# Performance work log

Measured on AMD Instinct MI355X. Metric: run time of the kernel, lower is better.

## Reference

```python
import jax, jax.numpy as jnp
import numpy as np

EULER = 0.5772156649015329  # Euler-Mascheroni constant


def _expi_neg(t):
    """Ei(t) for t < 0, via Ei(t) = -E1(-t).

    E1 uses the power series for x < 8 and the asymptotic expansion for x >= 8.
    This replaces the scipy.special.expi CPU round-trip of the original module.
    """
    x = -t  # x > 0
    # --- series branch (x < 8): E1(x) = -gamma - ln(x) + sum_{k>=1} (-1)^{k+1} x^k/(k*k!)
    xs = jnp.minimum(x, 8.0)
    s = jnp.zeros_like(xs)
    term = xs  # (-1)^{k+1} xs^k / k!  starting at k=1
    for k in range(1, 31):
        s = s + term / k
        term = term * (-xs) / (k + 1)
    e1_small = -EULER - jnp.log(xs) + s
    # --- asymptotic branch (x >= 8): E1(x) ~ e^{-x}/x * sum_n (-1)^n n! / x^n
    xl = jnp.maximum(x, 8.0)
    a = jnp.ones_like(xl)
    acc = jnp.ones_like(xl)
    for n in range(1, 9):
        a = a * (-n) / xl
        acc = acc + a
    e1_large = jnp.exp(-xl) / xl * acc
    e1 = jnp.where(x < 8.0, e1_small, e1_large)
    return -e1


def _li(v):
    # logarithmic integral li(v) = Ei(ln v); constant w.r.t. params (scipy detaches in torch)
    return jax.lax.stop_gradient(_expi_neg(jnp.log(v)))


def _phi(u, var2, var3, var4, var5):
    log_term = jnp.log(1.0 - u)
    li_term = _li(1.0 - u)
    return (var2 / log_term
            + var3 * li_term
            + var4 * ((1.0 - u) / log_term - li_term)
            + var5 * ((1.0 - u) * (log_term + 1.0) / (2.0 * log_term ** 2) - li_term / 2.0))


def setup_inputs() -> dict:
    key = jax.random.key(0)
    B, L, D = 262144, 64, 32
    hidden = [128, 128, 64]
    ks = jax.random.split(key, 16)
    u = jax.random.uniform(ks[0], (B, L), dtype=jnp.float32, minval=1e-4, maxval=1.0 - 1e-4)
    dims = [L] + hidden + [D]
    inp = {"u": u}
    for i in range(4):
        inp[f"W{i}"] = jax.random.normal(ks[1 + 2 * i], (dims[i], dims[i + 1]), dtype=jnp.float32) / np.sqrt(dims[i]).astype(np.float32)
        inp[f"b{i}"] = jnp.zeros((dims[i + 1],), dtype=jnp.float32)
    for j in range(1, 7):
        inp[f"var{j}"] = jax.random.normal(ks[8 + j], (1, D), dtype=jnp.float32) * 0.1
    return inp


def reference(u, W0, b0, W1, b1, W2, b2, W3, b3, var1, var2, var3, var4, var5, var6):
    # MLP: three Linear+ReLU blocks then final Linear to dim_data
    h = u
    for W, b in ((W0, b0), (W1, b1), (W2, b2)):
        h = jax.nn.relu(h @ W + b)
    net = h @ W3 + b3  # (B, dim_data)
    D = net.shape[1]
    ud = u[:, :D]
    # spline corrections
    p01 = -4.0 * ud ** 5 + 5.0 * ud ** 4
    corr1 = jnp.nan_to_num(p01 * (var1 + _phi(ud, var2, var3, var4, var5)), nan=0.0)
    corr2 = var6 * (ud ** 3 - 2.0 * ud ** 2 + ud)
    net_tif = jax.nn.relu(net + corr1 + corr2)
    # inverse TIF activation: ((1 - u^2)/2)^{-x}
    return jnp.power((1.0 - ud ** 2) / 2.0, -net_tif)
```

## Files before the change

### kernel.cpp

```cpp
#include <hip/hip_runtime.h>
#include <hip/hip_bf16.h>
#include <math.h>

#define PITCH_H 136
#define LN2_F 0.69314718055994531f

typedef _Float16 half8 __attribute__((ext_vector_type(8)));
typedef __attribute__((ext_vector_type(4))) float f32x4;
typedef __attribute__((ext_vector_type(8))) short short8;

__global__ void prep_weights(const float* __restrict__ W0, const float* __restrict__ W1,
                             const float* __restrict__ W2, const float* __restrict__ W3,
                             short* __restrict__ ws) {
    int e = blockIdx.x * 256 + threadIdx.x;
    const float* W; int N, NT, base, ul;
    if (e < 1024)      { W = W0; N = 128; NT = 8; base = 0;     ul = e; }
    else if (e < 3072) { W = W1; N = 128; NT = 8; base = 8192;  ul = e - 1024; }
    else if (e < 4096) { W = W2; N = 64;  NT = 4; base = 24576; ul = e - 3072; }
    else if (e < 4352) { W = W3; N = 32;  NT = 2; base = 32768; ul = e - 4096; }
    else return;
    const int cp = ul >> 6, lane = ul & 63;
    const int s = cp / NT, ct = cp % NT;
    const int k0 = s * 32 + (lane >> 4) * 8;
    const int n = ct * 16 + (lane & 15);
    union { half8 h; short8 s; } v;
#pragma unroll
    for (int j = 0; j < 8; ++j) v.h[j] = (_Float16)W[(size_t)(k0 + j) * N + n];
    *(short8*)(ws + base + cp * 512 + lane * 8) = v.s;
}

template <int K, int N>
__device__ __forceinline__ void layer_frag2(const half8* __restrict__ wf,
                                            const float* __restrict__ bias,
                                            const half8 (&af)[2][4], int lane, int m,
                                            f32x4 (&acc)[2][8]) {
    constexpr int NK = K / 32, NT = N / 16;
#pragma unroll
    for (int ct = 0; ct < NT; ++ct) {
        float b = bias[ct * 16 + m];
        acc[0][ct] = f32x4{b, b, b, b};
        acc[1][ct] = f32x4{b, b, b, b};
    }
#pragma unroll
    for (int s = 0; s < NK; ++s) {
#pragma unroll
        for (int ct = 0; ct < NT; ++ct) {
            half8 bh = wf[(size_t)(s * NT + ct) * 64 + lane];
            acc[0][ct] = __builtin_amdgcn_mfma_f32_16x16x32_f16(af[0][s], bh, acc[0][ct], 0, 0, 0);
            acc[1][ct] = __builtin_amdgcn_mfma_f32_16x16x32_f16(af[1][s], bh, acc[1][ct], 0, 0, 0);
        }
    }
}

template <int K>
__device__ __forceinline__ void load_a_lds(const _Float16* __restrict__ lw, int m, int q,
                                           half8 af[4]) {
    const _Float16* rp = lw + m * PITCH_H + q * 8;
#pragma unroll
    for (int s = 0; s < K / 32; ++s) af[s] = *(const half8*)(rp + s * 32);
}

template <int N>
__device__ __forceinline__ void store_d_lds(_Float16* __restrict__ lw, int m, int q,
                                            const f32x4* acc, bool relu) {
#pragma unroll
    for (int ct = 0; ct < N / 16; ++ct) {
#pragma unroll
        for (int r = 0; r < 4; ++r) {
            float v = acc[ct][r];
            if (relu) v = fmaxf(v, 0.0f);
            lw[(q * 4 + r) * PITCH_H + ct * 16 + m] = (_Float16)v;
        }
    }
}

__global__ __launch_bounds__(256, 2) void mlp_phi_mfma(
    const float* __restrict__ u,
    const float* __restrict__ b0, const float* __restrict__ b1,
    const float* __restrict__ b2, const float* __restrict__ b3,
    const short* __restrict__ ws,
    const float* __restrict__ var1, const float* __restrict__ var2,
    const float* __restrict__ var3, const float* __restrict__ var4,
    const float* __restrict__ var5, const float* __restrict__ var6,
    float* __restrict__ out) {
    __shared__ __align__(16) _Float16 lds[4 * 32 * PITCH_H];
    const int t = threadIdx.x, lane = t & 63, wave = t >> 6;
    const int m = lane & 15, q = lane >> 4;
    _Float16* lw = lds + wave * 32 * PITCH_H;
    const size_t row0 = (size_t)blockIdx.x * 128 + wave * 32;

    const half8* wf0 = (const half8*)(ws);
    const half8* wf1 = (const half8*)(ws + 8192);
    const half8* wf2 = (const half8*)(ws + 24576);
    const half8* wf3 = (const half8*)(ws + 32768);

    half8 af[2][4];
    f32x4 acc[2][8];

#pragma unroll
    for (int mt = 0; mt < 2; ++mt) {
        const float* up = u + (row0 + mt * 16 + m) * 64;
#pragma unroll
        for (int s = 0; s < 2; ++s) {
            float4 v0 = *(const float4*)(up + s * 32 + q * 8);
            float4 v1 = *(const float4*)(up + s * 32 + q * 8 + 4);
            half8 a;
            a[0] = (_Float16)v0.x; a[1] = (_Float16)v0.y;
            a[2] = (_Float16)v0.z; a[3] = (_Float16)v0.w;
            a[4] = (_Float16)v1.x; a[5] = (_Float16)v1.y;
            a[6] = (_Float16)v1.z; a[7] = (_Float16)v1.w;
            af[mt][s] = a;
        }
    }
    layer_frag2<64, 128>(wf0, b0, af, lane, m, acc);
#pragma unroll
    for (int mt = 0; mt < 2; ++mt) store_d_lds<128>(lw + mt * 16 * PITCH_H, m, q, acc[mt], true);

#pragma unroll
    for (int mt = 0; mt < 2; ++mt) load_a_lds<128>(lw + mt * 16 * PITCH_H, m, q, af[mt]);
    layer_frag2<128, 128>(wf1, b1, af, lane, m, acc);
#pragma unroll
    for (int mt = 0; mt < 2; ++mt) store_d_lds<128>(lw + mt * 16 * PITCH_H, m, q, acc[mt], true);

#pragma unroll
    for (int mt = 0; mt < 2; ++mt) load_a_lds<128>(lw + mt * 16 * PITCH_H, m, q, af[mt]);
    layer_frag2<128, 64>(wf2, b2, af, lane, m, acc);
#pragma unroll
    for (int mt = 0; mt < 2; ++mt) store_d_lds<64>(lw + mt * 16 * PITCH_H, m, q, acc[mt], true);

#pragma unroll
    for (int mt = 0; mt < 2; ++mt) load_a_lds<64>(lw + mt * 16 * PITCH_H, m, q, af[mt]);

    float ue[2][8];
#pragma unroll
    for (int mt = 0; mt < 2; ++mt)
#pragma unroll
        for (int ot = 0; ot < 2; ++ot)
#pragma unroll
            for (int r = 0; r < 4; ++r)
                ue[mt][ot * 4 + r] = u[(row0 + mt * 16 + q * 4 + r) * 64 + ot * 16 + m];

    layer_frag2<64, 32>(wf3, b3, af, lane, m, acc);

#pragma unroll
    for (int ot = 0; ot < 2; ++ot) {
        const int d = ot * 16 + m;
        const float v1 = var1[d], v2 = var2[d], v3 = var3[d],
                    v4 = var4[d], v6 = var6[d];
        const float v5h = 0.5f * var5[d];
        const float c3 = v3 - v4 - v5h;
#pragma unroll
        for (int mt = 0; mt < 2; ++mt) {
#pragma unroll
            for (int r = 0; r < 4; ++r) {
                const size_t row = row0 + mt * 16 + q * 4 + r;
                const float net = acc[mt][ot][r];
                const float ud = ue[mt][ot * 4 + r];

                const float omu = 1.0f - ud;
                const float lt = __log2f(omu) * LN2_F;
                const float x = -lt;

                const float e1s = -__log2f(x) * LN2_F
                    + (-0.57721566f + x * (0.99999193f + x * (-0.24991055f
                    + x * (0.05519968f + x * (-0.00976004f + x * 0.00107857f)))));
                const float num = 0.2677737343f + x * (8.6347608925f + x * (18.0590169730f
                    + x * (8.5733287401f + x)));
                const float den = 3.9584969228f + x * (21.0996530827f + x * (25.6329561486f
                    + x * (9.5733223454f + x)));
                const float e1l = __expf(-x) * num * __builtin_amdgcn_rcpf(x * den);
                const float li = -((x < 1.0f) ? e1s : e1l);

                const float rl = __builtin_amdgcn_rcpf(lt);
                const float phi = fmaf(v4, omu, v2) * rl
                                + (v5h * omu * (lt + 1.0f)) * rl * rl
                                + c3 * li;

                const float ud2 = ud * ud;
                const float ud4 = ud2 * ud2;
                const float p01 = ud4 * fmaf(-4.0f, ud, 5.0f);
                const float corr1 = p01 * (v1 + phi);
                const float d1 = ud - 1.0f;
                const float corr2 = v6 * ud * d1 * d1;

                const float nt = fmaxf(net + corr1 + corr2, 0.0f);
                const float base = fmaf(-0.5f, ud2, 0.5f);
                out[row * 32 + d] = __builtin_amdgcn_exp2f(-nt * __log2f(base));
            }
        }
    }
}

extern "C" void kernel_launch(void* const* d_in, const int* in_sizes, int n_in,
                              void* d_out, int out_size, void* d_ws, size_t ws_size,
                              hipStream_t stream) {
    const float* u    = (const float*)d_in[0];
    const float* W0   = (const float*)d_in[1];
    const float* b0   = (const float*)d_in[2];
    const float* W1   = (const float*)d_in[3];
    const float* b1   = (const float*)d_in[4];
    const float* W2   = (const float*)d_in[5];
    const float* b2   = (const float*)d_in[6];
    const float* W3   = (const float*)d_in[7];
    const float* b3   = (const float*)d_in[8];
    const float* var1 = (const float*)d_in[9];
    const float* var2 = (const float*)d_in[10];
    const float* var3 = (const float*)d_in[11];
    const float* var4 = (const float*)d_in[12];
    const float* var5 = (const float*)d_in[13];
    const float* var6 = (const float*)d_in[14];
    float* out = (float*)d_out;
    short* ws = (short*)d_ws;

    prep_weights<<<dim3(17), dim3(256), 0, stream>>>(W0, W1, W2, W3, ws);

    const int B = in_sizes[0] / 64;
    const int blocks = B / 128;
    mlp_phi_mfma<<<dim3(blocks), dim3(256), 0, stream>>>(
        u, b0, b1, b2, b3, ws,
        var1, var2, var3, var4, var5, var6, out);
}
```

Baseline: 158.4 us.

## Stage fp16 weights in LDS with persistent 512-thread blocks

Converts the kernel to a persistent grid of up to 256 blocks of 512 threads that loop over 256-row chunks. Each block copies the prepacked fp16 weights into LDS once and hoists biases and var-derived constants into registers, so MFMA B-fragments are read from LDS instead of global/L2 on every tile. LDS use rises to about 139 KB per block, which can allow only one block per CU and caps the grid at 256 blocks. That limits occupancy and latency hiding, and the weight copy is a fixed startup cost per block.

```diff
diff --git a/kernel.cpp b/kernel.cpp
--- a/kernel.cpp
+++ b/kernel.cpp
@@ -4,6 +4,10 @@
 
 #define PITCH_H 136
 #define LN2_F 0.69314718055994531f
+#define WS_SHORTS 34816
+#define WS_BYTES  69632
+#define ACT_BYTES (8 * 32 * PITCH_H * 2)
+#define LDS_TOTAL (WS_BYTES + ACT_BYTES)
 
 typedef _Float16 half8 __attribute__((ext_vector_type(8)));
 typedef __attribute__((ext_vector_type(4))) float f32x4;
@@ -30,14 +34,14 @@
 }
 
 template <int K, int N>
-__device__ __forceinline__ void layer_frag2(const half8* __restrict__ wf,
-                                            const float* __restrict__ bias,
-                                            const half8 (&af)[2][4], int lane, int m,
+__device__ __forceinline__ void layer_frag2(const half8* wf,
+                                            const float* bias,
+                                            const half8 (&af)[2][4], int lane,
                                             f32x4 (&acc)[2][8]) {
     constexpr int NK = K / 32, NT = N / 16;
 #pragma unroll
     for (int ct = 0; ct < NT; ++ct) {
-        float b = bias[ct * 16 + m];
+        float b = bias[ct];
         acc[0][ct] = f32x4{b, b, b, b};
         acc[1][ct] = f32x4{b, b, b, b};
     }
@@ -45,7 +49,7 @@
     for (int s = 0; s < NK; ++s) {
 #pragma unroll
         for (int ct = 0; ct < NT; ++ct) {
-            half8 bh = wf[(size_t)(s * NT + ct) * 64 + lane];
+            half8 bh = wf[(s * NT + ct) * 64 + lane];
             acc[0][ct] = __builtin_amdgcn_mfma_f32_16x16x32_f16(af[0][s], bh, acc[0][ct], 0, 0, 0);
             acc[1][ct] = __builtin_amdgcn_mfma_f32_16x16x32_f16(af[1][s], bh, acc[1][ct], 0, 0, 0);
         }
@@ -74,7 +78,7 @@
     }
 }
 
-__global__ __launch_bounds__(256, 2) void mlp_phi_mfma(
+__global__ __launch_bounds__(512, 2) void mlp_phi_mfma(
     const float* __restrict__ u,
     const float* __restrict__ b0, const float* __restrict__ b1,
     const float* __restrict__ b2, const float* __restrict__ b3,
@@ -82,110 +86,141 @@
     const float* __restrict__ var1, const float* __restrict__ var2,
     const float* __restrict__ var3, const float* __restrict__ var4,
     const float* __restrict__ var5, const float* __restrict__ var6,
-    float* __restrict__ out) {
-    __shared__ __align__(16) _Float16 lds[4 * 32 * PITCH_H];
+    float* __restrict__ out, int nchunks) {
+    extern __shared__ __align__(16) char smem[];
+    short* wsl = (short*)smem;
+    _Float16* act = (_Float16*)(smem + WS_BYTES);
+
     const int t = threadIdx.x, lane = t & 63, wave = t >> 6;
     const int m = lane & 15, q = lane >> 4;
-    _Float16* lw = lds + wave * 32 * PITCH_H;
-    const size_t row0 = (size_t)blockIdx.x * 128 + wave * 32;
-
-    const half8* wf0 = (const half8*)(ws);
-    const half8* wf1 = (const half8*)(ws + 8192);
-    const half8* wf2 = (const half8*)(ws + 24576);
-    const half8* wf3 = (const half8*)(ws + 32768);
+
+#pragma unroll 1
+    for (int i = t; i < WS_SHORTS / 8; i += 512)
+        ((short8*)wsl)[i] = ((const short8*)ws)[i];
+
+    float bb0[8], bb1[8], bb2[4], bb3[2];
+#pragma unroll
+    for (int ct = 0; ct < 8; ++ct) bb0[ct] = b0[ct * 16 + m];
+#pragma unroll
+    for (int ct = 0; ct < 8; ++ct) bb1[ct] = b1[ct * 16 + m];
+#pragma unroll
+    for (int ct = 0; ct < 4; ++ct) bb2[ct] = b2[ct * 16 + m];
+#pragma unroll
+    for (int ct = 0; ct < 2; ++ct) bb3[ct] = b3[ct * 16 + m];
+
+    float ev1[2], ev2[2], ev4[2], ev6[2], ev5h[2], ec3[2];
+#pragma unroll
+    for (int ot = 0; ot < 2; ++ot) {
+        const int d = ot * 16 + m;
+        ev1[ot] = var1[d]; ev2[ot] = var2[d]; ev4[ot] = var4[d]; ev6[ot] = var6[d];
+        ev5h[ot] = 0.5f * var5[d];
+        ec3[ot] = var3[d] - ev4[ot] - ev5h[ot];
+    }
+
+    __syncthreads();
+
+    const half8* wf0 = (const half8*)(wsl);
+    const half8* wf1 = (const half8*)(wsl + 8192);
+    const half8* wf2 = (const half8*)(wsl + 24576);
+    const half8* wf3 = (const half8*)(wsl + 32768);
+    _Float16* lw = act + wave * 32 * PITCH_H;
 
     half8 af[2][4];
     f32x4 acc[2][8];
 
-#pragma unroll
-    for (int mt = 0; mt < 2; ++mt) {
-        const float* up = u + (row0 + mt * 16 + m) * 64;
-#pragma unroll
-        for (int s = 0; s < 2; ++s) {
-            float4 v0 = *(const float4*)(up + s * 32 + q * 8);
-            float4 v1 = *(const float4*)(up + s * 32 + q * 8 + 4);
-            half8 a;
-            a[0] = (_Float16)v0.x; a[1] = (_Float16)v0.y;
-            a[2] = (_Float16)v0.z; a[3] = (_Float16)v0.w;
-            a[4] = (_Float16)v1.x; a[5] = (_Float16)v1.y;
-            a[6] = (_Float16)v1.z; a[7] = (_Float16)v1.w;
-            af[mt][s] = a;
-        }
-    }
-    layer_frag2<64, 128>(wf0, b0, af, lane, m, acc);
-#pragma unroll
-    for (int mt = 0; mt < 2; ++mt) store_d_lds<128>(lw + mt * 16 * PITCH_H, m, q, acc[mt], true);
-
-#pragma unroll
-    for (int mt = 0; mt < 2; ++mt) load_a_lds<128>(lw + mt * 16 * PITCH_H, m, q, af[mt]);
-    layer_frag2<128, 128>(wf1, b1, af, lane, m, acc);
-#pragma unroll
-    for (int mt = 0; mt < 2; ++mt) store_d_lds<128>(lw + mt * 16 * PITCH_H, m, q, acc[mt], true);
-
-#pragma unroll
-    for (int mt = 0; mt < 2; ++mt) load_a_lds<128>(lw + mt * 16 * PITCH_H, m, q, af[mt]);
-    layer_frag2<128, 64>(wf2, b2, af, lane, m, acc);
-#pragma unroll
-    for (int mt = 0; mt < 2; ++mt) store_d_lds<64>(lw + mt * 16 * PITCH_H, m, q, acc[mt], true);
-
-#pragma unroll
-    for (int mt = 0; mt < 2; ++mt) load_a_lds<64>(lw + mt * 16 * PITCH_H, m, q, af[mt]);
-
-    float ue[2][8];
-#pragma unroll
-    for (int mt = 0; mt < 2; ++mt)
-#pragma unroll
-        for (int ot = 0; ot < 2; ++ot)
-#pragma unroll
-            for (int r = 0; r < 4; ++r)
-                ue[mt][ot * 4 + r] = u[(row0 + mt * 16 + q * 4 + r) * 64 + ot * 16 + m];
-
-    layer_frag2<64, 32>(wf3, b3, af, lane, m, acc);
-
-#pragma unroll
-    for (int ot = 0; ot < 2; ++ot) {
-        const int d = ot * 16 + m;
-        const float v1 = var1[d], v2 = var2[d], v3 = var3[d],
-                    v4 = var4[d], v6 = var6[d];
-        const float v5h = 0.5f * var5[d];
-        const float c3 = v3 - v4 - v5h;
+#pragma unroll 1
+    for (int c = blockIdx.x; c < nchunks; c += gridDim.x) {
+        const size_t row0 = (size_t)c * 256 + wave * 32;
+
 #pragma unroll
         for (int mt = 0; mt < 2; ++mt) {
-#pragma unroll
-            for (int r = 0; r < 4; ++r) {
-                const size_t row = row0 + mt * 16 + q * 4 + r;
-                const float net = acc[mt][ot][r];
-                const float ud = ue[mt][ot * 4 + r];
-
-                const float omu = 1.0f - ud;
-                const float lt = __log2f(omu) * LN2_F;
-                const float x = -lt;
-
-                const float e1s = -__log2f(x) * LN2_F
-                    + (-0.57721566f + x * (0.99999193f + x * (-0.24991055f
-                    + x * (0.05519968f + x * (-0.00976004f + x * 0.00107857f)))));
-                const float num = 0.2677737343f + x * (8.6347608925f + x * (18.0590169730f
-                    + x * (8.5733287401f + x)));
-                const float den = 3.9584969228f + x * (21.0996530827f + x * (25.6329561486f
-                    + x * (9.5733223454f + x)));
-                const float e1l = __expf(-x) * num * __builtin_amdgcn_rcpf(x * den);
-                const float li = -((x < 1.0f) ? e1s : e1l);
-
-                const float rl = __builtin_amdgcn_rcpf(lt);
-                const float phi = fmaf(v4, omu, v2) * rl
-                                + (v5h * omu * (lt + 1.0f)) * rl * rl
-                                + c3 * li;
-
-                const float ud2 = ud * ud;
-                const float ud4 = ud2 * ud2;
-                const float p01 = ud4 * fmaf(-4.0f, ud, 5.0f);
-                const float corr1 = p01 * (v1 + phi);
-                const float d1 = ud - 1.0f;
-                const float corr2 = v6 * ud * d1 * d1;
-
-                const float nt = fmaxf(net + corr1 + corr2, 0.0f);
-                const float base = fmaf(-0.5f, ud2, 0.5f);
-                out[row * 32 + d] = __builtin_amdgcn_exp2f(-nt * __log2f(base));
+            const float* up = u + (row0 + mt * 16 + m) * 64;
+#pragma unroll
+            for (int s = 0; s < 2; ++s) {
+                float4 v0 = *(const float4*)(up + s * 32 + q * 8);
+                float4 v1 = *(const float4*)(up + s * 32 + q * 8 + 4);
+                half8 a;
+                a[0] = (_Float16)v0.x; a[1] = (_Float16)v0.y;
+                a[2] = (_Float16)v0.z; a[3] = (_Float16)v0.w;
+                a[4] = (_Float16)v1.x; a[5] = (_Float16)v1.y;
+                a[6] = (_Float16)v1.z; a[7] = (_Float16)v1.w;
+                af[mt][s] = a;
+            }
+        }
+        layer_frag2<64, 128>(wf0, bb0, af, lane, acc);
+#pragma unroll
+        for (int mt = 0; mt < 2; ++mt) store_d_lds<128>(lw + mt * 16 * PITCH_H, m, q, acc[mt], true);
+
+#pragma unroll
+        for (int mt = 0; mt < 2; ++mt) load_a_lds<128>(lw + mt * 16 * PITCH_H, m, q, af[mt]);
+        layer_frag2<128, 128>(wf1, bb1, af, lane, acc);
+#pragma unroll
+        for (int mt = 0; mt < 2; ++mt) store_d_lds<128>(lw + mt * 16 * PITCH_H, m, q, acc[mt], true);
+
+#pragma unroll
+        for (int mt = 0; mt < 2; ++mt) load_a_lds<128>(lw + mt * 16 * PITCH_H, m, q, af[mt]);
+        layer_frag2<128, 64>(wf2, bb2, af, lane, acc);
+#pragma unroll
+        for (int mt = 0; mt < 2; ++mt) store_d_lds<64>(lw + mt * 16 * PITCH_H, m, q, acc[mt], true);
+
+#pragma unroll
+        for (int mt = 0; mt < 2; ++mt) load_a_lds<64>(lw + mt * 16 * PITCH_H, m, q, af[mt]);
+
+        float ue[2][8];
+#pragma unroll
+        for (int mt = 0; mt < 2; ++mt)
+#pragma unroll
+            for (int ot = 0; ot < 2; ++ot)
+#pragma unroll
+                for (int r = 0; r < 4; ++r)
+                    ue[mt][ot * 4 + r] = u[(row0 + mt * 16 + q * 4 + r) * 64 + ot * 16 + m];
+
+        layer_frag2<64, 32>(wf3, bb3, af, lane, acc);
+
+#pragma unroll
+        for (int ot = 0; ot < 2; ++ot) {
+            const int d = ot * 16 + m;
+            const float v1 = ev1[ot], v2 = ev2[ot], v4 = ev4[ot], v6 = ev6[ot];
+            const float v5h = ev5h[ot];
+            const float c3 = ec3[ot];
+#pragma unroll
+            for (int mt = 0; mt < 2; ++mt) {
+#pragma unroll
+                for (int r = 0; r < 4; ++r) {
+                    const size_t row = row0 + mt * 16 + q * 4 + r;
+                    const float net = acc[mt][ot][r];
+                    const float ud = ue[mt][ot * 4 + r];
+
+                    const float omu = 1.0f - ud;
+                    const float lt = __log2f(omu) * LN2_F;
+                    const float x = -lt;
+
+                    const float e1s = -__log2f(x) * LN2_F
+                        + (-0.57721566f + x * (0.99999193f + x * (-0.24991055f
+                        + x * (0.05519968f + x * (-0.00976004f + x * 0.00107857f)))));
+                    const float num = 0.2677737343f + x * (8.6347608925f + x * (18.0590169730f
+                        + x * (8.5733287401f + x)));
+                    const float den = 3.9584969228f + x * (21.0996530827f + x * (25.6329561486f
+                        + x * (9.5733223454f + x)));
+                    const float e1l = __expf(-x) * num * __builtin_amdgcn_rcpf(x * den);
+                    const float li = -((x < 1.0f) ? e1s : e1l);
+
+                    const float rl = __builtin_amdgcn_rcpf(lt);
+                    const float phi = fmaf(v4, omu, v2) * rl
+                                    + (v5h * omu * (lt + 1.0f)) * rl * rl
+                                    + c3 * li;
+
+                    const float ud2 = ud * ud;
+                    const float ud4 = ud2 * ud2;
+                    const float p01 = ud4 * fmaf(-4.0f, ud, 5.0f);
+                    const float corr1 = p01 * (v1 + phi);
+                    const float d1 = ud - 1.0f;
+                    const float corr2 = v6 * ud * d1 * d1;
+
+                    const float nt = fmaxf(net + corr1 + corr2, 0.0f);
+                    const float base = fmaf(-0.5f, ud2, 0.5f);
+                    out[row * 32 + d] = __builtin_amdgcn_exp2f(-nt * __log2f(base));
+                }
             }
         }
     }
@@ -214,9 +249,13 @@
 
     prep_weights<<<dim3(17), dim3(256), 0, stream>>>(W0, W1, W2, W3, ws);
 
+    hipFuncSetAttribute(reinterpret_cast<const void*>(mlp_phi_mfma),
+                        hipFuncAttributeMaxDynamicSharedMemorySize, LDS_TOTAL);
+
     const int B = in_sizes[0] / 64;
-    const int blocks = B / 128;
-    mlp_phi_mfma<<<dim3(blocks), dim3(256), 0, stream>>>(
+    const int nchunks = B / 256;
+    const int nblocks = nchunks < 256 ? nchunks : 256;
+    mlp_phi_mfma<<<dim3(nblocks), dim3(512), LDS_TOTAL, stream>>>(
         u, b0, b1, b2, b3, ws,
-        var1, var2, var3, var4, var5, var6, out);
-}
+        var1, var2, var3, var4, var5, var6, out, nchunks);
+}
```

New measurement: 150.2 us. -5.2%, faster.

## Use transposed LDS reads, double-buffered weight prefetch, and higher occupancy

Applied to the files above, without the earlier changes.

Swaps the padded row-major LDS staging between layers for a fragment-blocked layout that is read back with ds_read_b64_tr_b16, so each lane gets its A fragment from packed 64-bit stores and transposed loads rather than scalar half stores. Weight fragments are now prefetched one K-step ahead into two register buffers, and biases and spline parameters are loaded once at kernel start. Float-to-half conversion uses packed cvt_pkrtz, which rounds toward zero instead of to nearest. Launch bounds move from 2 to 4 blocks per CU, which caps register use and may cause spills given the larger register footprint.

```diff
diff --git a/kernel.cpp b/kernel.cpp
--- a/kernel.cpp
+++ b/kernel.cpp
@@ -2,10 +2,11 @@
 #include <hip/hip_bf16.h>
 #include <math.h>
 
-#define PITCH_H 136
 #define LN2_F 0.69314718055994531f
 
 typedef _Float16 half8 __attribute__((ext_vector_type(8)));
+typedef _Float16 h4_t __attribute__((ext_vector_type(4)));
+typedef __fp16 pk2_t __attribute__((ext_vector_type(2)));
 typedef __attribute__((ext_vector_type(4))) float f32x4;
 typedef __attribute__((ext_vector_type(8))) short short8;
 
@@ -29,52 +30,83 @@
     *(short8*)(ws + base + cp * 512 + lane * 8) = v.s;
 }
 
+#define REGION_HALFS 2048
+
+__device__ __forceinline__ void lds_fence() {
+    asm volatile("s_waitcnt lgkmcnt(0)" ::: "memory");
+}
+
+template <int K>
+__device__ __forceinline__ void load_a_tr(const _Float16* region, unsigned lane_off,
+                                          half8 af[4]) {
+    const unsigned base = (unsigned)(uintptr_t)region + lane_off;
+#pragma unroll
+    for (int s = 0; s < K / 32; ++s) {
+        h4_t lo, hi;
+        asm volatile("ds_read_b64_tr_b16 %0, %2\n\t"
+                     "ds_read_b64_tr_b16 %1, %2 offset:128"
+                     : "=&v"(lo), "=&v"(hi)
+                     : "v"(base + (unsigned)(s * 1024))
+                     : "memory");
+        af[s] = __builtin_shufflevector(lo, hi, 0, 1, 2, 3, 4, 5, 6, 7);
+    }
+}
+
+template <int N>
+__device__ __forceinline__ void store_d_tr(_Float16* __restrict__ region, int m, int q,
+                                           const f32x4* acc, bool relu) {
+    const int base = (m >> 2) * 64 + (m & 3) * 16 + q * 4;
+#pragma unroll
+    for (int ct = 0; ct < N / 16; ++ct) {
+        f32x4 v = acc[ct];
+        float a0 = relu ? fmaxf(v[0], 0.0f) : v[0];
+        float a1 = relu ? fmaxf(v[1], 0.0f) : v[1];
+        float a2 = relu ? fmaxf(v[2], 0.0f) : v[2];
+        float a3 = relu ? fmaxf(v[3], 0.0f) : v[3];
+        pk2_t p0 = __builtin_amdgcn_cvt_pkrtz(a0, a1);
+        pk2_t p1 = __builtin_amdgcn_cvt_pkrtz(a2, a3);
+        h4_t h = {(_Float16)p0[0], (_Float16)p0[1], (_Float16)p1[0], (_Float16)p1[1]};
+        *(h4_t*)(region + ct * 256 + base) = h;
+    }
+}
+
+template <int NT>
+__device__ __forceinline__ void preload_b(const half8* __restrict__ wf, int lane,
+                                          half8 (&b)[8]) {
+#pragma unroll
+    for (int ct = 0; ct < NT; ++ct) b[ct] = wf[ct * 64 + lane];
+}
+
 template <int K, int N>
 __device__ __forceinline__ void layer_frag2(const half8* __restrict__ wf,
-                                            const float* __restrict__ bias,
-                                            const half8 (&af)[2][4], int lane, int m,
-                                            f32x4 (&acc)[2][8]) {
+                                            const float* bias,
+                                            const half8 (&af)[2][4], int lane,
+                                            f32x4 (&acc)[2][8],
+                                            half8 (&ba)[8], half8 (&bb)[8]) {
     constexpr int NK = K / 32, NT = N / 16;
 #pragma unroll
     for (int ct = 0; ct < NT; ++ct) {
-        float b = bias[ct * 16 + m];
+        float b = bias[ct];
         acc[0][ct] = f32x4{b, b, b, b};
         acc[1][ct] = f32x4{b, b, b, b};
     }
 #pragma unroll
     for (int s = 0; s < NK; ++s) {
+        half8 (&bc)[8] = (s & 1) ? bb : ba;
+        half8 (&bn)[8] = (s & 1) ? ba : bb;
+        if (s + 1 < NK) {
+#pragma unroll
+            for (int ct = 0; ct < NT; ++ct) bn[ct] = wf[((s + 1) * NT + ct) * 64 + lane];
+        }
 #pragma unroll
         for (int ct = 0; ct < NT; ++ct) {
-            half8 bh = wf[(size_t)(s * NT + ct) * 64 + lane];
-            acc[0][ct] = __builtin_amdgcn_mfma_f32_16x16x32_f16(af[0][s], bh, acc[0][ct], 0, 0, 0);
-            acc[1][ct] = __builtin_amdgcn_mfma_f32_16x16x32_f16(af[1][s], bh, acc[1][ct], 0, 0, 0);
-        }
-    }
-}
-
-template <int K>
-__device__ __forceinline__ void load_a_lds(const _Float16* __restrict__ lw, int m, int q,
-                                           half8 af[4]) {
-    const _Float16* rp = lw + m * PITCH_H + q * 8;
-#pragma unroll
-    for (int s = 0; s < K / 32; ++s) af[s] = *(const half8*)(rp + s * 32);
-}
-
-template <int N>
-__device__ __forceinline__ void store_d_lds(_Float16* __restrict__ lw, int m, int q,
-                                            const f32x4* acc, bool relu) {
-#pragma unroll
-    for (int ct = 0; ct < N / 16; ++ct) {
-#pragma unroll
-        for (int r = 0; r < 4; ++r) {
-            float v = acc[ct][r];
-            if (relu) v = fmaxf(v, 0.0f);
-            lw[(q * 4 + r) * PITCH_H + ct * 16 + m] = (_Float16)v;
-        }
-    }
-}
-
-__global__ __launch_bounds__(256, 2) void mlp_phi_mfma(
+            acc[0][ct] = __builtin_amdgcn_mfma_f32_16x16x32_f16(af[0][s], bc[ct], acc[0][ct], 0, 0, 0);
+            acc[1][ct] = __builtin_amdgcn_mfma_f32_16x16x32_f16(af[1][s], bc[ct], acc[1][ct], 0, 0, 0);
+        }
+    }
+}
+
+__global__ __launch_bounds__(256, 4) void mlp_phi_mfma(
     const float* __restrict__ u,
     const float* __restrict__ b0, const float* __restrict__ b1,
     const float* __restrict__ b2, const float* __restrict__ b3,
@@ -83,10 +115,11 @@
     const float* __restrict__ var3, const float* __restrict__ var4,
     const float* __restrict__ var5, const float* __restrict__ var6,
     float* __restrict__ out) {
-    __shared__ __align__(16) _Float16 lds[4 * 32 * PITCH_H];
+    __shared__ __align__(16) _Float16 lds[4 * 2 * REGION_HALFS];
     const int t = threadIdx.x, lane = t & 63, wave = t >> 6;
     const int m = lane & 15, q = lane >> 4;
-    _Float16* lw = lds + wave * 32 * PITCH_H;
+    _Float16* lw = lds + wave * 2 * REGION_HALFS;
+    const unsigned lane_rd = (unsigned)(q * 256 + m * 8);
     const size_t row0 = (size_t)blockIdx.x * 128 + wave * 32;
 
     const half8* wf0 = (const half8*)(ws);
@@ -94,8 +127,28 @@
     const half8* wf2 = (const half8*)(ws + 24576);
     const half8* wf3 = (const half8*)(ws + 32768);
 
+    float bb0v[8], bb1v[8], bb2v[4], bb3v[2];
+#pragma unroll
+    for (int ct = 0; ct < 8; ++ct) bb0v[ct] = b0[ct * 16 + m];
+#pragma unroll
+    for (int ct = 0; ct < 8; ++ct) bb1v[ct] = b1[ct * 16 + m];
+#pragma unroll
+    for (int ct = 0; ct < 4; ++ct) bb2v[ct] = b2[ct * 16 + m];
+#pragma unroll
+    for (int ct = 0; ct < 2; ++ct) bb3v[ct] = b3[ct * 16 + m];
+
+    float ev1[2], ev2[2], ev4[2], ev6[2], ev5h[2], ec3[2];
+#pragma unroll
+    for (int ot = 0; ot < 2; ++ot) {
+        const int d = ot * 16 + m;
+        ev1[ot] = var1[d]; ev2[ot] = var2[d]; ev4[ot] = var4[d]; ev6[ot] = var6[d];
+        ev5h[ot] = 0.5f * var5[d];
+        ec3[ot] = var3[d] - ev4[ot] - ev5h[ot];
+    }
+
     half8 af[2][4];
     f32x4 acc[2][8];
+    half8 ba[8], bb[8];
 
 #pragma unroll
     for (int mt = 0; mt < 2; ++mt) {
@@ -104,32 +157,43 @@
         for (int s = 0; s < 2; ++s) {
             float4 v0 = *(const float4*)(up + s * 32 + q * 8);
             float4 v1 = *(const float4*)(up + s * 32 + q * 8 + 4);
-            half8 a;
-            a[0] = (_Float16)v0.x; a[1] = (_Float16)v0.y;
-            a[2] = (_Float16)v0.z; a[3] = (_Float16)v0.w;
-            a[4] = (_Float16)v1.x; a[5] = (_Float16)v1.y;
-            a[6] = (_Float16)v1.z; a[7] = (_Float16)v1.w;
-            af[mt][s] = a;
-        }
-    }
-    layer_frag2<64, 128>(wf0, b0, af, lane, m, acc);
-#pragma unroll
-    for (int mt = 0; mt < 2; ++mt) store_d_lds<128>(lw + mt * 16 * PITCH_H, m, q, acc[mt], true);
-
-#pragma unroll
-    for (int mt = 0; mt < 2; ++mt) load_a_lds<128>(lw + mt * 16 * PITCH_H, m, q, af[mt]);
-    layer_frag2<128, 128>(wf1, b1, af, lane, m, acc);
-#pragma unroll
-    for (int mt = 0; mt < 2; ++mt) store_d_lds<128>(lw + mt * 16 * PITCH_H, m, q, acc[mt], true);
-
-#pragma unroll
-    for (int mt = 0; mt < 2; ++mt) load_a_lds<128>(lw + mt * 16 * PITCH_H, m, q, af[mt]);
-    layer_frag2<128, 64>(wf2, b2, af, lane, m, acc);
-#pragma unroll
-    for (int mt = 0; mt < 2; ++mt) store_d_lds<64>(lw + mt * 16 * PITCH_H, m, q, acc[mt], true);
-
-#pragma unroll
-    for (int mt = 0; mt < 2; ++mt) load_a_lds<64>(lw + mt * 16 * PITCH_H, m, q, af[mt]);
+            pk2_t p0 = __builtin_amdgcn_cvt_pkrtz(v0.x, v0.y);
+            pk2_t p1 = __builtin_amdgcn_cvt_pkrtz(v0.z, v0.w);
+            pk2_t p2 = __builtin_amdgcn_cvt_pkrtz(v1.x, v1.y);
+            pk2_t p3 = __builtin_amdgcn_cvt_pkrtz(v1.z, v1.w);
+            af[mt][s] = half8{(_Float16)p0[0], (_Float16)p0[1], (_Float16)p1[0], (_Float16)p1[1],
+                              (_Float16)p2[0], (_Float16)p2[1], (_Float16)p3[0], (_Float16)p3[1]};
+        }
+    }
+    preload_b<8>(wf0, lane, ba);
+    layer_frag2<64, 128>(wf0, bb0v, af, lane, acc, ba, bb);
+#pragma unroll
+    for (int mt = 0; mt < 2; ++mt) store_d_tr<128>(lw + mt * REGION_HALFS, m, q, acc[mt], true);
+
+    preload_b<8>(wf1, lane, ba);
+    lds_fence();
+    load_a_tr<128>(lw, lane_rd, af[0]);
+    load_a_tr<128>(lw + REGION_HALFS, lane_rd, af[1]);
+    lds_fence();
+    __builtin_amdgcn_sched_barrier(0);
+    layer_frag2<128, 128>(wf1, bb1v, af, lane, acc, ba, bb);
+#pragma unroll
+    for (int mt = 0; mt < 2; ++mt) store_d_tr<128>(lw + mt * REGION_HALFS, m, q, acc[mt], true);
+
+    preload_b<4>(wf2, lane, ba);
+    lds_fence();
+    load_a_tr<128>(lw, lane_rd, af[0]);
+    load_a_tr<128>(lw + REGION_HALFS, lane_rd, af[1]);
+    lds_fence();
+    __builtin_amdgcn_sched_barrier(0);
+    layer_frag2<128, 64>(wf2, bb2v, af, lane, acc, ba, bb);
+#pragma unroll
+    for (int mt = 0; mt < 2; ++mt) store_d_tr<64>(lw + mt * REGION_HALFS, m, q, acc[mt], true);
+
+    preload_b<2>(wf3, lane, ba);
+    lds_fence();
+    load_a_tr<64>(lw, lane_rd, af[0]);
+    load_a_tr<64>(lw + REGION_HALFS, lane_rd, af[1]);
 
     float ue[2][8];
 #pragma unroll
@@ -140,15 +204,16 @@
             for (int r = 0; r < 4; ++r)
                 ue[mt][ot * 4 + r] = u[(row0 + mt * 16 + q * 4 + r) * 64 + ot * 16 + m];
 
-    layer_frag2<64, 32>(wf3, b3, af, lane, m, acc);
+    lds_fence();
+    __builtin_amdgcn_sched_barrier(0);
+    layer_frag2<64, 32>(wf3, bb3v, af, lane, acc, ba, bb);
 
 #pragma unroll
     for (int ot = 0; ot < 2; ++ot) {
         const int d = ot * 16 + m;
-        const float v1 = var1[d], v2 = var2[d], v3 = var3[d],
-                    v4 = var4[d], v6 = var6[d];
-        const float v5h = 0.5f * var5[d];
-        const float c3 = v3 - v4 - v5h;
+        const float v1 = ev1[ot], v2 = ev2[ot], v4 = ev4[ot], v6 = ev6[ot];
+        const float v5h = ev5h[ot];
+        const float c3 = ec3[ot];
 #pragma unroll
         for (int mt = 0; mt < 2; ++mt) {
 #pragma unroll
```

Result: slower. 175.9 us (+11.0%).

## Keep weight slices in registers with persistent grid and column-split waves

Applied to the files above, without the earlier changes.

Restructures the MLP kernel so each wave owns a fixed slice of output columns and holds its slice of all four weight matrices in registers. A persistent grid of up to 1024 blocks loops over 32-row chunks, which removes the per-block weight reloads from global memory. Activations pass between layers through LDS with a tiled layout read by transposing ds_read_b64_tr_b16 loads. The cost is three block-wide barriers per layer step and less per-wave work to hide latency, since the four waves now split columns of the same rows.

```diff
diff --git a/kernel.cpp b/kernel.cpp
--- a/kernel.cpp
+++ b/kernel.cpp
@@ -2,10 +2,12 @@
 #include <hip/hip_bf16.h>
 #include <math.h>
 
-#define PITCH_H 136
 #define LN2_F 0.69314718055994531f
+#define REGION_HALFS 2048
 
 typedef _Float16 half8 __attribute__((ext_vector_type(8)));
+typedef _Float16 h4_t __attribute__((ext_vector_type(4)));
+typedef __fp16 pk2_t __attribute__((ext_vector_type(2)));
 typedef __attribute__((ext_vector_type(4))) float f32x4;
 typedef __attribute__((ext_vector_type(8))) short short8;
 
@@ -29,49 +31,32 @@
     *(short8*)(ws + base + cp * 512 + lane * 8) = v.s;
 }
 
-template <int K, int N>
-__device__ __forceinline__ void layer_frag2(const half8* __restrict__ wf,
-                                            const float* __restrict__ bias,
-                                            const half8 (&af)[2][4], int lane, int m,
-                                            f32x4 (&acc)[2][8]) {
-    constexpr int NK = K / 32, NT = N / 16;
-#pragma unroll
-    for (int ct = 0; ct < NT; ++ct) {
-        float b = bias[ct * 16 + m];
-        acc[0][ct] = f32x4{b, b, b, b};
-        acc[1][ct] = f32x4{b, b, b, b};
-    }
-#pragma unroll
-    for (int s = 0; s < NK; ++s) {
-#pragma unroll
-        for (int ct = 0; ct < NT; ++ct) {
-            half8 bh = wf[(size_t)(s * NT + ct) * 64 + lane];
-            acc[0][ct] = __builtin_amdgcn_mfma_f32_16x16x32_f16(af[0][s], bh, acc[0][ct], 0, 0, 0);
-            acc[1][ct] = __builtin_amdgcn_mfma_f32_16x16x32_f16(af[1][s], bh, acc[1][ct], 0, 0, 0);
-        }
-    }
-}
-
-template <int K>
-__device__ __forceinline__ void load_a_lds(const _Float16* __restrict__ lw, int m, int q,
-                                           half8 af[4]) {
-    const _Float16* rp = lw + m * PITCH_H + q * 8;
-#pragma unroll
-    for (int s = 0; s < K / 32; ++s) af[s] = *(const half8*)(rp + s * 32);
-}
-
-template <int N>
-__device__ __forceinline__ void store_d_lds(_Float16* __restrict__ lw, int m, int q,
-                                            const f32x4* acc, bool relu) {
-#pragma unroll
-    for (int ct = 0; ct < N / 16; ++ct) {
-#pragma unroll
-        for (int r = 0; r < 4; ++r) {
-            float v = acc[ct][r];
-            if (relu) v = fmaxf(v, 0.0f);
-            lw[(q * 4 + r) * PITCH_H + ct * 16 + m] = (_Float16)v;
-        }
-    }
+
+__device__ __forceinline__ void lds_fence() {
+    asm volatile("s_waitcnt lgkmcnt(0)" ::: "memory");
+}
+
+__device__ __forceinline__ half8 tr_read_ks(const _Float16* region, unsigned lane_off, int s) {
+    h4_t lo, hi;
+    asm volatile("ds_read_b64_tr_b16 %0, %2\n\t"
+                 "ds_read_b64_tr_b16 %1, %2 offset:128"
+                 : "=&v"(lo), "=&v"(hi)
+                 : "v"((unsigned)(uintptr_t)region + lane_off + (unsigned)(s * 1024))
+                 : "memory");
+    return __builtin_shufflevector(lo, hi, 0, 1, 2, 3, 4, 5, 6, 7);
+}
+
+__device__ __forceinline__ void store_tile(_Float16* __restrict__ region, int ct_global,
+                                           int m, int q, f32x4 v, bool relu) {
+    const int base = ct_global * 256 + (m >> 2) * 64 + (m & 3) * 16 + q * 4;
+    float a0 = relu ? fmaxf(v[0], 0.0f) : v[0];
+    float a1 = relu ? fmaxf(v[1], 0.0f) : v[1];
+    float a2 = relu ? fmaxf(v[2], 0.0f) : v[2];
+    float a3 = relu ? fmaxf(v[3], 0.0f) : v[3];
+    pk2_t p0 = __builtin_amdgcn_cvt_pkrtz(a0, a1);
+    pk2_t p1 = __builtin_amdgcn_cvt_pkrtz(a2, a3);
+    h4_t h = {(_Float16)p0[0], (_Float16)p0[1], (_Float16)p1[0], (_Float16)p1[1]};
+    *(h4_t*)(region + base) = h;
 }
 
 __global__ __launch_bounds__(256, 2) void mlp_phi_mfma(
@@ -82,112 +67,180 @@
     const float* __restrict__ var1, const float* __restrict__ var2,
     const float* __restrict__ var3, const float* __restrict__ var4,
     const float* __restrict__ var5, const float* __restrict__ var6,
-    float* __restrict__ out) {
-    __shared__ __align__(16) _Float16 lds[4 * 32 * PITCH_H];
+    float* __restrict__ out, int nchunks) {
+    __shared__ __align__(16) _Float16 bufA[2 * REGION_HALFS];
+    __shared__ __align__(16) _Float16 bufB[2 * REGION_HALFS];
     const int t = threadIdx.x, lane = t & 63, wave = t >> 6;
     const int m = lane & 15, q = lane >> 4;
-    _Float16* lw = lds + wave * 32 * PITCH_H;
-    const size_t row0 = (size_t)blockIdx.x * 128 + wave * 32;
+    const unsigned lane_rd = (unsigned)(q * 256 + m * 8);
+    const int ct01 = 2 * wave;
+    const int mt3 = wave >> 1, ct3 = wave & 1;
 
     const half8* wf0 = (const half8*)(ws);
     const half8* wf1 = (const half8*)(ws + 8192);
     const half8* wf2 = (const half8*)(ws + 24576);
     const half8* wf3 = (const half8*)(ws + 32768);
 
-    half8 af[2][4];
-    f32x4 acc[2][8];
-
-#pragma unroll
-    for (int mt = 0; mt < 2; ++mt) {
-        const float* up = u + (row0 + mt * 16 + m) * 64;
-#pragma unroll
-        for (int s = 0; s < 2; ++s) {
-            float4 v0 = *(const float4*)(up + s * 32 + q * 8);
-            float4 v1 = *(const float4*)(up + s * 32 + q * 8 + 4);
-            half8 a;
-            a[0] = (_Float16)v0.x; a[1] = (_Float16)v0.y;
-            a[2] = (_Float16)v0.z; a[3] = (_Float16)v0.w;
-            a[4] = (_Float16)v1.x; a[5] = (_Float16)v1.y;
-            a[6] = (_Float16)v1.z; a[7] = (_Float16)v1.w;
-            af[mt][s] = a;
-        }
+    half8 w0f[2][2], w1f[4][2], w2f[4], w3f[2];
+#pragma unroll
+    for (int s = 0; s < 2; ++s)
+#pragma unroll
+        for (int cl = 0; cl < 2; ++cl)
+            w0f[s][cl] = wf0[(s * 8 + ct01 + cl) * 64 + lane];
+#pragma unroll
+    for (int s = 0; s < 4; ++s)
+#pragma unroll
+        for (int cl = 0; cl < 2; ++cl)
+            w1f[s][cl] = wf1[(s * 8 + ct01 + cl) * 64 + lane];
+#pragma unroll
+    for (int s = 0; s < 4; ++s) w2f[s] = wf2[(s * 4 + wave) * 64 + lane];
+#pragma unroll
+    for (int s = 0; s < 2; ++s) w3f[s] = wf3[(s * 2 + ct3) * 64 + lane];
+
+    float bias0[2], bias1[2];
+#pragma unroll
+    for (int cl = 0; cl < 2; ++cl) {
+        bias0[cl] = b0[(ct01 + cl) * 16 + m];
+        bias1[cl] = b1[(ct01 + cl) * 16 + m];
     }
-    layer_frag2<64, 128>(wf0, b0, af, lane, m, acc);
-#pragma unroll
-    for (int mt = 0; mt < 2; ++mt) store_d_lds<128>(lw + mt * 16 * PITCH_H, m, q, acc[mt], true);
-
-#pragma unroll
-    for (int mt = 0; mt < 2; ++mt) load_a_lds<128>(lw + mt * 16 * PITCH_H, m, q, af[mt]);
-    layer_frag2<128, 128>(wf1, b1, af, lane, m, acc);
-#pragma unroll
-    for (int mt = 0; mt < 2; ++mt) store_d_lds<128>(lw + mt * 16 * PITCH_H, m, q, acc[mt], true);
-
-#pragma unroll
-    for (int mt = 0; mt < 2; ++mt) load_a_lds<128>(lw + mt * 16 * PITCH_H, m, q, af[mt]);
-    layer_frag2<128, 64>(wf2, b2, af, lane, m, acc);
-#pragma unroll
-    for (int mt = 0; mt < 2; ++mt) store_d_lds<64>(lw + mt * 16 * PITCH_H, m, q, acc[mt], true);
-
-#pragma unroll
-    for (int mt = 0; mt < 2; ++mt) load_a_lds<64>(lw + mt * 16 * PITCH_H, m, q, af[mt]);
-
-    float ue[2][8];
-#pragma unroll
-    for (int mt = 0; mt < 2; ++mt)
-#pragma unroll
-        for (int ot = 0; ot < 2; ++ot)
-#pragma unroll
-            for (int r = 0; r < 4; ++r)
-                ue[mt][ot * 4 + r] = u[(row0 + mt * 16 + q * 4 + r) * 64 + ot * 16 + m];
-
-    layer_frag2<64, 32>(wf3, b3, af, lane, m, acc);
-
-#pragma unroll
-    for (int ot = 0; ot < 2; ++ot) {
-        const int d = ot * 16 + m;
-        const float v1 = var1[d], v2 = var2[d], v3 = var3[d],
-                    v4 = var4[d], v6 = var6[d];
-        const float v5h = 0.5f * var5[d];
-        const float c3 = v3 - v4 - v5h;
+    const float bias2 = b2[wave * 16 + m];
+    const float bias3 = b3[ct3 * 16 + m];
+
+    const int d = ct3 * 16 + m;
+    const float v1 = var1[d], v2 = var2[d], v4 = var4[d], v6 = var6[d];
+    const float v5h = 0.5f * var5[d];
+    const float c3 = var3[d] - v4 - v5h;
+
+    f32x4 acc[2][2];
+
+#pragma unroll 1
+    for (int c = blockIdx.x; c < nchunks; c += gridDim.x) {
+        const size_t row0 = (size_t)c * 32;
+
 #pragma unroll
         for (int mt = 0; mt < 2; ++mt) {
-#pragma unroll
-            for (int r = 0; r < 4; ++r) {
-                const size_t row = row0 + mt * 16 + q * 4 + r;
-                const float net = acc[mt][ot][r];
-                const float ud = ue[mt][ot * 4 + r];
-
-                const float omu = 1.0f - ud;
-                const float lt = __log2f(omu) * LN2_F;
-                const float x = -lt;
-
-                const float e1s = -__log2f(x) * LN2_F
-                    + (-0.57721566f + x * (0.99999193f + x * (-0.24991055f
-                    + x * (0.05519968f + x * (-0.00976004f + x * 0.00107857f)))));
-                const float num = 0.2677737343f + x * (8.6347608925f + x * (18.0590169730f
-                    + x * (8.5733287401f + x)));
-                const float den = 3.9584969228f + x * (21.0996530827f + x * (25.6329561486f
-                    + x * (9.5733223454f + x)));
-                const float e1l = __expf(-x) * num * __builtin_amdgcn_rcpf(x * den);
-                const float li = -((x < 1.0f) ? e1s : e1l);
-
-                const float rl = __builtin_amdgcn_rcpf(lt);
-                const float phi = fmaf(v4, omu, v2) * rl
-                                + (v5h * omu * (lt + 1.0f)) * rl * rl
-                                + c3 * li;
-
-                const float ud2 = ud * ud;
-                const float ud4 = ud2 * ud2;
-                const float p01 = ud4 * fmaf(-4.0f, ud, 5.0f);
-                const float corr1 = p01 * (v1 + phi);
-                const float d1 = ud - 1.0f;
-                const float corr2 = v6 * ud * d1 * d1;
-
-                const float nt = fmaxf(net + corr1 + corr2, 0.0f);
-                const float base = fmaf(-0.5f, ud2, 0.5f);
-                out[row * 32 + d] = __builtin_amdgcn_exp2f(-nt * __log2f(base));
+            const float* up = u + (row0 + mt * 16 + m) * 64;
+            half8 a0[2];
+#pragma unroll
+            for (int s = 0; s < 2; ++s) {
+                float4 v0a = *(const float4*)(up + s * 32 + q * 8);
+                float4 v1a = *(const float4*)(up + s * 32 + q * 8 + 4);
+                pk2_t p0 = __builtin_amdgcn_cvt_pkrtz(v0a.x, v0a.y);
+                pk2_t p1 = __builtin_amdgcn_cvt_pkrtz(v0a.z, v0a.w);
+                pk2_t p2 = __builtin_amdgcn_cvt_pkrtz(v1a.x, v1a.y);
+                pk2_t p3 = __builtin_amdgcn_cvt_pkrtz(v1a.z, v1a.w);
+                a0[s] = half8{(_Float16)p0[0], (_Float16)p0[1], (_Float16)p1[0], (_Float16)p1[1],
+                              (_Float16)p2[0], (_Float16)p2[1], (_Float16)p3[0], (_Float16)p3[1]};
             }
-        }
+#pragma unroll
+            for (int cl = 0; cl < 2; ++cl) {
+                float b = bias0[cl];
+                acc[mt][cl] = f32x4{b, b, b, b};
+            }
+#pragma unroll
+            for (int s = 0; s < 2; ++s)
+#pragma unroll
+                for (int cl = 0; cl < 2; ++cl)
+                    acc[mt][cl] = __builtin_amdgcn_mfma_f32_16x16x32_f16(a0[s], w0f[s][cl],
+                                                                         acc[mt][cl], 0, 0, 0);
+#pragma unroll
+            for (int cl = 0; cl < 2; ++cl)
+                store_tile(bufA + mt * REGION_HALFS, ct01 + cl, m, q, acc[mt][cl], true);
+        }
+        __syncthreads();
+
+#pragma unroll
+        for (int mt = 0; mt < 2; ++mt) {
+            half8 af[4];
+#pragma unroll
+            for (int s = 0; s < 4; ++s) af[s] = tr_read_ks(bufA + mt * REGION_HALFS, lane_rd, s);
+            lds_fence();
+            __builtin_amdgcn_sched_barrier(0);
+#pragma unroll
+            for (int cl = 0; cl < 2; ++cl) {
+                float b = bias1[cl];
+                acc[mt][cl] = f32x4{b, b, b, b};
+            }
+#pragma unroll
+            for (int s = 0; s < 4; ++s)
+#pragma unroll
+                for (int cl = 0; cl < 2; ++cl)
+                    acc[mt][cl] = __builtin_amdgcn_mfma_f32_16x16x32_f16(af[s], w1f[s][cl],
+                                                                         acc[mt][cl], 0, 0, 0);
+#pragma unroll
+            for (int cl = 0; cl < 2; ++cl)
+                store_tile(bufB + mt * REGION_HALFS, ct01 + cl, m, q, acc[mt][cl], true);
+        }
+        __syncthreads();
+
+        f32x4 acc2[2];
+#pragma unroll
+        for (int mt = 0; mt < 2; ++mt) {
+            half8 af[4];
+#pragma unroll
+            for (int s = 0; s < 4; ++s) af[s] = tr_read_ks(bufB + mt * REGION_HALFS, lane_rd, s);
+            lds_fence();
+            __builtin_amdgcn_sched_barrier(0);
+            acc2[mt] = f32x4{bias2, bias2, bias2, bias2};
+#pragma unroll
+            for (int s = 0; s < 4; ++s)
+                acc2[mt] = __builtin_amdgcn_mfma_f32_16x16x32_f16(af[s], w2f[s], acc2[mt], 0, 0, 0);
+            store_tile(bufA + mt * REGION_HALFS, wave, m, q, acc2[mt], true);
+        }
+        __syncthreads();
+
+        half8 a3[2];
+#pragma unroll
+        for (int s = 0; s < 2; ++s) a3[s] = tr_read_ks(bufA + mt3 * REGION_HALFS, lane_rd, s);
+
+        float ue[4];
+#pragma unroll
+        for (int r = 0; r < 4; ++r)
+            ue[r] = u[(row0 + mt3 * 16 + q * 4 + r) * 64 + d];
+
+        lds_fence();
+        __builtin_amdgcn_sched_barrier(0);
+        f32x4 acc3 = f32x4{bias3, bias3, bias3, bias3};
+        acc3 = __builtin_amdgcn_mfma_f32_16x16x32_f16(a3[0], w3f[0], acc3, 0, 0, 0);
+        acc3 = __builtin_amdgcn_mfma_f32_16x16x32_f16(a3[1], w3f[1], acc3, 0, 0, 0);
+
+#pragma unroll
+        for (int r = 0; r < 4; ++r) {
+            const size_t row = row0 + mt3 * 16 + q * 4 + r;
+            const float net = acc3[r];
+            const float ud = ue[r];
+
+            const float omu = 1.0f - ud;
+            const float lt = __log2f(omu) * LN2_F;
+            const float x = -lt;
+
+            const float e1s = -__log2f(x) * LN2_F
+                + (-0.57721566f + x * (0.99999193f + x * (-0.24991055f
+                + x * (0.05519968f + x * (-0.00976004f + x * 0.00107857f)))));
+            const float num = 0.2677737343f + x * (8.6347608925f + x * (18.0590169730f
+                + x * (8.5733287401f + x)));
+            const float den = 3.9584969228f + x * (21.0996530827f + x * (25.6329561486f
+                + x * (9.5733223454f + x)));
+            const float e1l = __expf(-x) * num * __builtin_amdgcn_rcpf(x * den);
+            const float li = -((x < 1.0f) ? e1s : e1l);
+
+            const float rl = __builtin_amdgcn_rcpf(lt);
+            const float phi = fmaf(v4, omu, v2) * rl
+                            + (v5h * omu * (lt + 1.0f)) * rl * rl
+                            + c3 * li;
+
+            const float ud2 = ud * ud;
+            const float ud4 = ud2 * ud2;
+            const float p01 = ud4 * fmaf(-4.0f, ud, 5.0f);
+            const float corr1 = p01 * (v1 + phi);
+            const float d1 = ud - 1.0f;
+            const float corr2 = v6 * ud * d1 * d1;
+
+            const float nt = fmaxf(net + corr1 + corr2, 0.0f);
+            const float base = fmaf(-0.5f, ud2, 0.5f);
+            out[row * 32 + d] = __builtin_amdgcn_exp2f(-nt * __log2f(base));
+        }
+        __syncthreads();
     }
 }
 
@@ -215,8 +268,9 @@
     prep_weights<<<dim3(17), dim3(256), 0, stream>>>(W0, W1, W2, W3, ws);
 
     const int B = in_sizes[0] / 64;
-    const int blocks = B / 128;
-    mlp_phi_mfma<<<dim3(blocks), dim3(256), 0, stream>>>(
+    const int nchunks = B / 32;
+    const int nblocks = nchunks < 1024 ? nchunks : 1024;
+    mlp_phi_mfma<<<dim3(nblocks), dim3(256), 0, stream>>>(
         u, b0, b1, b2, b3, ws,
-        var1, var2, var3, var4, var5, var6, out);
-}
+        var1, var2, var3, var4, var5, var6, out, nchunks);
+}
```

Measured after the change: 173.1 us. 1.09x slower.
